# Kernel optimization log

Hardware: AMD Instinct MI355X
Metric: run time of the kernel (lower is better)

Reference implementation:

```python
import jax, jax.numpy as jnp
import numpy as np

# LocBlock.get_obj_matrix, fully vectorized over batch B and points N.
# Per point i: Q_e[c,c]=w_i*kron(m_i m_i^T, I3), Q_e[t,t]=w_i*I3,
# Q_e[h,h]=w_i*y_i^T y_i, Q_e[c,t]=-w_i*kron(m_i, I3), Q_e[c,h]=-w_i*kron(m_i, y_i),
# Q_e[t,h]=w_i*y_i; summed over i, then offset removed and Frobenius-normalized.

B, N = 1024, 4096

def setup_inputs() -> dict:
    key = jax.random.key(0)
    k1, k2, k3 = jax.random.split(key, 3)
    return {
        "keypoints_3D_src": jax.random.normal(k1, (B, 3, N), dtype=jnp.float32),
        "keypoints_3D_trg": jax.random.normal(k2, (B, 3, N), dtype=jnp.float32),
        "weights": jax.random.uniform(k3, (B, 1, N), dtype=jnp.float32),
    }


def reference(keypoints_3D_src, keypoints_3D_trg, weights):
    m = keypoints_3D_src              # (B,3,N) source points
    y = keypoints_3D_trg              # (B,3,N) target points
    w = weights[:, 0, :]              # (B,N) per-point scalar weights
    b = m.shape[0]
    I3 = jnp.eye(3, dtype=m.dtype)

    # weighted moment sums over points
    Mw = jnp.einsum('bin,bjn,bn->bij', m, m, w)          # (B,3,3) sum w m m^T
    mw = jnp.einsum('bin,bn->bi', m, w)                  # (B,3)   sum w m
    yw = jnp.einsum('bin,bn->bi', y, w)                  # (B,3)   sum w y
    MY = jnp.einsum('bin,bjn,bn->bij', m, y, w)          # (B,3,3) sum w m y^T
    sw = jnp.sum(w, axis=-1)                             # (B,)    sum w
    yy = jnp.einsum('bin,bin,bn->b', y, y, w)            # (B,)    sum w y^T y

    # assemble blocks (kron index convention: kron(A,B)[3i+k,3j+l]=A[ij]B[kl])
    Qcc = jnp.einsum('bij,kl->bikjl', Mw, I3).reshape(b, 9, 9)   # kron(Mw, I3)
    Qct = -jnp.einsum('bi,kl->bikl', mw, I3).reshape(b, 9, 3)    # -kron(mw, I3)
    Qch = -MY.reshape(b, 9)                                      # -kron(m, W y) summed
    Qtt = sw[:, None, None] * I3                                 # (B,3,3)

    Q = jnp.zeros((b, 13, 13), dtype=m.dtype)
    Q = Q.at[:, 1:10, 1:10].set(Qcc)
    Q = Q.at[:, 10:13, 10:13].set(Qtt)
    Q = Q.at[:, 1:10, 10:13].set(Qct)
    Q = Q.at[:, 10:13, 1:10].set(jnp.swapaxes(Qct, 1, 2))
    Q = Q.at[:, 1:10, 0].set(Qch)
    Q = Q.at[:, 0, 1:10].set(Qch)
    Q = Q.at[:, 10:13, 0].set(yw)
    Q = Q.at[:, 0, 10:13].set(yw)
    # Q[0,0] would be yy (offset); original zeroes it before normalization
    offsets = yy
    scales = jnp.sqrt(jnp.sum(Q * Q, axis=(1, 2)))  # Frobenius norm with Q[0,0]=0
    Qn = Q / scales[:, None, None]
    return Qn, scales, offsets
```

## Files before the change

kernel.cpp:

```cpp
#include <hip/hip_runtime.h>
#include <math.h>

#define BATCH    1024
#define NPTS     4096
#define THREADS  256
#define WAVES    (THREADS / 64)
#define SPLITS   2
#define SLICE    (NPTS / SPLITS)
#define SLICE_V  (SLICE / 4)
#define ITERS    (SLICE_V / THREADS)
#define NACC     23
#define WS_STRIDE 24

typedef float fx4 __attribute__((ext_vector_type(4)));


__device__ inline fx4 nt_load4(const float* p) {
    return __builtin_nontemporal_load((const fx4*)p);
}

__global__ __launch_bounds__(THREADS) void locblock_stage1(
    const float* __restrict__ m,
    const float* __restrict__ y,
    const float* __restrict__ w,
    float* __restrict__ ws)
{
    const int blk  = blockIdx.x;
    const int b    = blk >> 1;
    const int s    = blk & 1;
    const int tid  = threadIdx.x;
    const int lane = tid & 63;
    const int wave = tid >> 6;

    const size_t mb  = (size_t)b * 3 * NPTS;
    const int    off = s * SLICE;
    const float* m0p = m + mb + 0 * NPTS + off;
    const float* m1p = m + mb + 1 * NPTS + off;
    const float* m2p = m + mb + 2 * NPTS + off;
    const float* y0p = y + mb + 0 * NPTS + off;
    const float* y1p = y + mb + 1 * NPTS + off;
    const float* y2p = y + mb + 2 * NPTS + off;
    const float* wp  = w + (size_t)b * NPTS + off;

    float acc[NACC];
#pragma unroll
    for (int i = 0; i < NACC; ++i) acc[i] = 0.f;

    auto accum = [&](float wv, float m0v, float m1v, float m2v,
                     float y0v, float y1v, float y2v) {
        float wm0 = wv * m0v, wm1 = wv * m1v, wm2 = wv * m2v;
        acc[0]  += wv;
        acc[1]  += wm0;        acc[2]  += wm1;        acc[3]  += wm2;
        acc[4]  += wv * y0v;   acc[5]  += wv * y1v;   acc[6]  += wv * y2v;
        acc[7]  += wm0 * m0v;  acc[8]  += wm0 * m1v;  acc[9]  += wm0 * m2v;
        acc[10] += wm1 * m1v;  acc[11] += wm1 * m2v;  acc[12] += wm2 * m2v;
        acc[13] += wm0 * y0v;  acc[14] += wm0 * y1v;  acc[15] += wm0 * y2v;
        acc[16] += wm1 * y0v;  acc[17] += wm1 * y1v;  acc[18] += wm1 * y2v;
        acc[19] += wm2 * y0v;  acc[20] += wm2 * y1v;  acc[21] += wm2 * y2v;
        acc[22] += wv * (y0v * y0v + y1v * y1v + y2v * y2v);
    };

    fx4 M0[ITERS], M1[ITERS], M2[ITERS], Y0[ITERS], Y1[ITERS], Y2[ITERS], W[ITERS];
#pragma unroll
    for (int it = 0; it < ITERS; ++it) {
        const int v = (it * THREADS + tid) * 4;
        M0[it] = nt_load4(m0p + v); M1[it] = nt_load4(m1p + v); M2[it] = nt_load4(m2p + v);
        Y0[it] = nt_load4(y0p + v); Y1[it] = nt_load4(y1p + v); Y2[it] = nt_load4(y2p + v);
        W[it]  = nt_load4(wp + v);
    }
#pragma unroll
    for (int it = 0; it < ITERS; ++it) {
#pragma unroll
        for (int e = 0; e < 4; ++e) {
            accum(W[it][e], M0[it][e], M1[it][e], M2[it][e],
                  Y0[it][e], Y1[it][e], Y2[it][e]);
        }
    }

#pragma unroll
    for (int i = 0; i < NACC; ++i) {
        float v = acc[i];
        v += __shfl_xor(v, 32, 64);
        v += __shfl_xor(v, 16, 64);
        v += __shfl_xor(v, 8, 64);
        v += __shfl_xor(v, 4, 64);
        v += __shfl_xor(v, 2, 64);
        v += __shfl_xor(v, 1, 64);
        acc[i] = v;
    }

    __shared__ float partial[WAVES][NACC];
    if (lane == 0) {
#pragma unroll
        for (int i = 0; i < NACC; ++i) partial[wave][i] = acc[i];
    }
    __syncthreads();
    if (tid < NACC) {
        ws[(size_t)blk * WS_STRIDE + tid] =
            partial[0][tid] + partial[1][tid] + partial[2][tid] + partial[3][tid];
    }
}

__global__ __launch_bounds__(THREADS) void locblock_stage2(
    const float* __restrict__ ws,
    float* __restrict__ out)
{
    const int b    = blockIdx.x;
    const int tid  = threadIdx.x;
    const int lane = tid & 63;
    const int wave = tid >> 6;

    __shared__ float sums[NACC];
    __shared__ float red[WAVES];
    __shared__ float scale_s;

    if (tid < NACC) {
        float v = 0.f;
#pragma unroll
        for (int s = 0; s < SPLITS; ++s)
            v += ws[(size_t)(b * SPLITS + s) * WS_STRIDE + tid];
        sums[tid] = v;
    }
    __syncthreads();

    float qv = 0.f;
    if (tid < 169) {
        const int r = tid / 13, c = tid % 13;
        const float* mwv = &sums[1];
        const float* ywv = &sums[4];
        auto Mwf = [&](int i, int j) -> float {
            if (i > j) { int t = i; i = j; j = t; }
            int idx = (i == 0) ? j : ((i == 1) ? (j + 2) : 5);
            return sums[7 + idx];
        };
        auto MYf = [&](int i, int j) -> float { return sums[13 + i * 3 + j]; };

        if (r == 0) {
            if (c == 0)            qv = 0.f;
            else if (c <= 9)       qv = -MYf((c - 1) / 3, (c - 1) % 3);
            else                   qv = ywv[c - 10];
        } else if (c == 0) {
            if (r <= 9)            qv = -MYf((r - 1) / 3, (r - 1) % 3);
            else                   qv = ywv[r - 10];
        } else if (r <= 9 && c <= 9) {
            int a = r - 1, d = c - 1;
            int i = a / 3, k = a % 3, j = d / 3, l = d % 3;
            qv = (k == l) ? Mwf(i, j) : 0.f;
        } else if (r <= 9) {
            int a = r - 1, i = a / 3, k = a % 3, l = c - 10;
            qv = (k == l) ? -mwv[i] : 0.f;
        } else if (c <= 9) {
            int a = c - 1, i = a / 3, k = a % 3, l = r - 10;
            qv = (k == l) ? -mwv[i] : 0.f;
        } else {
            qv = (r == c) ? sums[0] : 0.f;
        }
    }

    float sq = (tid < 169) ? qv * qv : 0.f;
    sq += __shfl_xor(sq, 32, 64);
    sq += __shfl_xor(sq, 16, 64);
    sq += __shfl_xor(sq, 8, 64);
    sq += __shfl_xor(sq, 4, 64);
    sq += __shfl_xor(sq, 2, 64);
    sq += __shfl_xor(sq, 1, 64);
    if (lane == 0) red[wave] = sq;
    __syncthreads();
    if (tid == 0) {
        scale_s = sqrtf(red[0] + red[1] + red[2] + red[3]);
    }
    __syncthreads();

    const float inv_scale = 1.0f / scale_s;
    if (tid < 169) {
        out[(size_t)b * 169 + tid] = qv * inv_scale;
    }
    if (tid == 0) {
        out[(size_t)BATCH * 169 + b]         = scale_s;
        out[(size_t)BATCH * 169 + BATCH + b] = sums[22];
    }
}

extern "C" void kernel_launch(void* const* d_in, const int* in_sizes, int n_in,
                              void* d_out, int out_size, void* d_ws, size_t ws_size,
                              hipStream_t stream) {
    const float* m = (const float*)d_in[0];
    const float* y = (const float*)d_in[1];
    const float* w = (const float*)d_in[2];
    float* out = (float*)d_out;
    float* ws  = (float*)d_ws;

    locblock_stage1<<<BATCH * SPLITS, THREADS, 0, stream>>>(m, y, w, ws);
    locblock_stage2<<<BATCH, THREADS, 0, stream>>>(ws, out);
}
```

Before: 137.8 us.

## Fuse two-stage reduction into one kernel with one block per batch

Merges the partial-sum kernel and the matrix-assembly kernel into one launch. Each block now covers all points of a batch element, which removes the workspace round trip and the second launch. The cross-wave reduction now goes through a padded LDS transpose followed by wave-0 shuffles, loads become ordinary rather than nontemporal, and launch bounds ask for 3 blocks per CU. The trade-off is 1024 blocks instead of 2048, each holding twice as many registers' worth of loads in flight, so occupancy and latency hiding may suffer.

```diff
diff --git a/kernel.cpp b/kernel.cpp
--- a/kernel.cpp
+++ b/kernel.cpp
@@ -5,42 +5,46 @@
 #define NPTS     4096
 #define THREADS  256
 #define WAVES    (THREADS / 64)
-#define SPLITS   2
-#define SLICE    (NPTS / SPLITS)
-#define SLICE_V  (SLICE / 4)
-#define ITERS    (SLICE_V / THREADS)
+#define NV       (NPTS / 4)
+#define ITERS    (NV / THREADS)
 #define NACC     23
-#define WS_STRIDE 24
+#define RPAD     264
 
 typedef float fx4 __attribute__((ext_vector_type(4)));
 
 
-__device__ inline fx4 nt_load4(const float* p) {
-    return __builtin_nontemporal_load((const fx4*)p);
-}
-
-__global__ __launch_bounds__(THREADS) void locblock_stage1(
+__global__ __launch_bounds__(THREADS, 3) void locblock_fused(
     const float* __restrict__ m,
     const float* __restrict__ y,
     const float* __restrict__ w,
-    float* __restrict__ ws)
+    float* __restrict__ out)
 {
-    const int blk  = blockIdx.x;
-    const int b    = blk >> 1;
-    const int s    = blk & 1;
+    const int b    = blockIdx.x;
     const int tid  = threadIdx.x;
     const int lane = tid & 63;
     const int wave = tid >> 6;
 
-    const size_t mb  = (size_t)b * 3 * NPTS;
-    const int    off = s * SLICE;
-    const float* m0p = m + mb + 0 * NPTS + off;
-    const float* m1p = m + mb + 1 * NPTS + off;
-    const float* m2p = m + mb + 2 * NPTS + off;
-    const float* y0p = y + mb + 0 * NPTS + off;
-    const float* y1p = y + mb + 1 * NPTS + off;
-    const float* y2p = y + mb + 2 * NPTS + off;
-    const float* wp  = w + (size_t)b * NPTS + off;
+    const size_t mb = (size_t)b * 3 * NPTS;
+    const float* m0p = m + mb + 0 * NPTS;
+    const float* m1p = m + mb + 1 * NPTS;
+    const float* m2p = m + mb + 2 * NPTS;
+    const float* y0p = y + mb + 0 * NPTS;
+    const float* y1p = y + mb + 1 * NPTS;
+    const float* y2p = y + mb + 2 * NPTS;
+    const float* wp  = w + (size_t)b * NPTS;
+
+    fx4 M0[ITERS], M1[ITERS], M2[ITERS], Y0[ITERS], Y1[ITERS], Y2[ITERS], W[ITERS];
+#pragma unroll
+    for (int it = 0; it < ITERS; ++it) {
+        const int v = (it * THREADS + tid) * 4;
+        M0[it] = *(const fx4*)(m0p + v);
+        M1[it] = *(const fx4*)(m1p + v);
+        M2[it] = *(const fx4*)(m2p + v);
+        Y0[it] = *(const fx4*)(y0p + v);
+        Y1[it] = *(const fx4*)(y1p + v);
+        Y2[it] = *(const fx4*)(y2p + v);
+        W[it]  = *(const fx4*)(wp  + v);
+    }
 
     float acc[NACC];
 #pragma unroll
@@ -60,14 +64,6 @@
         acc[22] += wv * (y0v * y0v + y1v * y1v + y2v * y2v);
     };
 
-    fx4 M0[ITERS], M1[ITERS], M2[ITERS], Y0[ITERS], Y1[ITERS], Y2[ITERS], W[ITERS];
-#pragma unroll
-    for (int it = 0; it < ITERS; ++it) {
-        const int v = (it * THREADS + tid) * 4;
-        M0[it] = nt_load4(m0p + v); M1[it] = nt_load4(m1p + v); M2[it] = nt_load4(m2p + v);
-        Y0[it] = nt_load4(y0p + v); Y1[it] = nt_load4(y1p + v); Y2[it] = nt_load4(y2p + v);
-        W[it]  = nt_load4(wp + v);
-    }
 #pragma unroll
     for (int it = 0; it < ITERS; ++it) {
 #pragma unroll
@@ -77,49 +73,37 @@
         }
     }
 
-#pragma unroll
-    for (int i = 0; i < NACC; ++i) {
-        float v = acc[i];
-        v += __shfl_xor(v, 32, 64);
-        v += __shfl_xor(v, 16, 64);
-        v += __shfl_xor(v, 8, 64);
-        v += __shfl_xor(v, 4, 64);
-        v += __shfl_xor(v, 2, 64);
-        v += __shfl_xor(v, 1, 64);
-        acc[i] = v;
-    }
-
-    __shared__ float partial[WAVES][NACC];
-    if (lane == 0) {
-#pragma unroll
-        for (int i = 0; i < NACC; ++i) partial[wave][i] = acc[i];
-    }
-    __syncthreads();
-    if (tid < NACC) {
-        ws[(size_t)blk * WS_STRIDE + tid] =
-            partial[0][tid] + partial[1][tid] + partial[2][tid] + partial[3][tid];
-    }
-}
-
-__global__ __launch_bounds__(THREADS) void locblock_stage2(
-    const float* __restrict__ ws,
-    float* __restrict__ out)
-{
-    const int b    = blockIdx.x;
-    const int tid  = threadIdx.x;
-    const int lane = tid & 63;
-    const int wave = tid >> 6;
-
+    __shared__ float red_lds[NACC * RPAD];
     __shared__ float sums[NACC];
-    __shared__ float red[WAVES];
+    __shared__ float sqred[WAVES];
     __shared__ float scale_s;
 
-    if (tid < NACC) {
-        float v = 0.f;
 #pragma unroll
-        for (int s = 0; s < SPLITS; ++s)
-            v += ws[(size_t)(b * SPLITS + s) * WS_STRIDE + tid];
-        sums[tid] = v;
+    for (int i = 0; i < NACC; ++i) red_lds[i * RPAD + tid] = acc[i];
+    __syncthreads();
+
+    if (wave == 0) {
+        float part[NACC];
+#pragma unroll
+        for (int i = 0; i < NACC; ++i) {
+            const float* row = &red_lds[i * RPAD + lane];
+            part[i] = row[0] + row[64] + row[128] + row[192];
+        }
+#pragma unroll
+        for (int i = 0; i < NACC; ++i) {
+            float v = part[i];
+            v += __shfl_xor(v, 32, 64);
+            v += __shfl_xor(v, 16, 64);
+            v += __shfl_xor(v, 8, 64);
+            v += __shfl_xor(v, 4, 64);
+            v += __shfl_xor(v, 2, 64);
+            v += __shfl_xor(v, 1, 64);
+            part[i] = v;
+        }
+        if (lane == 0) {
+#pragma unroll
+            for (int i = 0; i < NACC; ++i) sums[i] = part[i];
+        }
     }
     __syncthreads();
 
@@ -164,10 +148,10 @@
     sq += __shfl_xor(sq, 4, 64);
     sq += __shfl_xor(sq, 2, 64);
     sq += __shfl_xor(sq, 1, 64);
-    if (lane == 0) red[wave] = sq;
+    if (lane == 0) sqred[wave] = sq;
     __syncthreads();
     if (tid == 0) {
-        scale_s = sqrtf(red[0] + red[1] + red[2] + red[3]);
+        scale_s = sqrtf(sqred[0] + sqred[1] + sqred[2] + sqred[3]);
     }
     __syncthreads();
 
@@ -188,8 +172,5 @@
     const float* y = (const float*)d_in[1];
     const float* w = (const float*)d_in[2];
     float* out = (float*)d_out;
-    float* ws  = (float*)d_ws;
-
-    locblock_stage1<<<BATCH * SPLITS, THREADS, 0, stream>>>(m, y, w, ws);
-    locblock_stage2<<<BATCH, THREADS, 0, stream>>>(ws, out);
+    locblock_fused<<<BATCH, THREADS, 0, stream>>>(m, y, w, out);
 }
```

After: 137.6 us. No clear change (-0.1%).
